# Kernel tuning notes

Measured on AMD Instinct MI355X. Metric: run time of the kernel, lower is better.

Reference implementation:

```python
import jax, jax.numpy as jnp
import numpy as np

N = 30000      # entities
E = 200000     # KG triples
E_ALL = 400000 # full-graph edges
R = 500        # relations
EH = 300       # e_hidden
RH = 100       # r_hidden
H = 8          # GAT / R2E heads
H_E2R = 2      # E2R heads: int(softmax(head_selector).sum()+1) == 2 always
EPS = 1e-16    # torch_geometric softmax eps


def _seg_softmax(logits, idx, num):
    # logits: [E, heads]; segment-wise stable softmax over edges grouped by idx
    m = jax.ops.segment_max(logits, idx, num_segments=num)
    ex = jnp.exp(logits - m[idx])
    s = jax.ops.segment_sum(ex, idx, num_segments=num)
    return ex / (s[idx] + EPS)


def _gcn(x, ei):
    j, i = ei[0], ei[1]
    deg = jax.ops.segment_sum(jnp.ones(ei.shape[1], x.dtype), i, num_segments=N)
    dis = jnp.where(deg > 0, deg ** -0.5, 0.0)
    norm = dis[j] * dis[i]                                        # [E_all]
    agg = jax.ops.segment_sum(norm[:, None] * x[j], i, num_segments=N)
    return jax.nn.relu(agg)


def _highway(x1, x2, w, b):
    gate = jax.nn.sigmoid(x1 @ w.T + b)
    return gate * x2 + (1.0 - gate) * x1


def setup_inputs() -> dict:
    key = jax.random.key(0)
    ks = jax.random.split(key, 20)
    f = jnp.float32
    inp = {
        'x_e': jax.random.normal(ks[0], (N, EH), f),
        'edge_index': jax.random.randint(ks[1], (2, E), 0, N),
        'rel': jax.random.randint(ks[2], (E,), 0, R),
        'edge_index_all': jax.random.randint(ks[3], (2, E_ALL), 0, N),
        'rel_all': jax.random.randint(ks[4], (E_ALL,), 0, R),
        # Highway layers
        'hw1_w': jax.random.normal(ks[5], (EH, EH), f) / np.sqrt(EH),
        'hw1_b': jnp.zeros((EH,), f),
        'hw2_w': jax.random.normal(ks[6], (EH, EH), f) / np.sqrt(EH),
        'hw2_b': jnp.zeros((EH,), f),
        # E2R (only first H_E2R heads are ever used)
        'e2r_wh': jax.random.normal(ks[7], (RH, EH), f) / np.sqrt(EH),
        'e2r_wt': jax.random.normal(ks[8], (RH, EH), f) / np.sqrt(EH),
        'e2r_ah': jax.random.normal(ks[9], (H_E2R, RH), f) / np.sqrt(RH),
        'e2r_at': jax.random.normal(ks[10], (H_E2R, RH), f) / np.sqrt(RH),
        # R2E
        'r2e_ah': jax.random.normal(ks[11], (H, EH), f) / np.sqrt(EH),
        'r2e_at': jax.random.normal(ks[12], (H, EH), f) / np.sqrt(EH),
        'r2e_ar': jax.random.normal(ks[13], (H, RH), f) / np.sqrt(RH),
        # GAT over e_hidden + 2*r_hidden = 500
        'gat_ai': jax.random.normal(ks[14], (H, EH + 2 * RH), f) / np.sqrt(EH + 2 * RH),
        'gat_aj': jax.random.normal(ks[15], (H, EH + 2 * RH), f) / np.sqrt(EH + 2 * RH),
    }
    return inp


def reference(x_e, edge_index, rel, edge_index_all, rel_all,
              hw1_w, hw1_b, hw2_w, hw2_b,
              e2r_wh, e2r_wt, e2r_ah, e2r_at,
              r2e_ah, r2e_at, r2e_ar, gat_ai, gat_aj):
    lrelu = jax.nn.leaky_relu  # slope 0.01, matches torch default

    # --- two GCN + Highway blocks (dropout = identity at eval) ---
    x = _highway(x_e, _gcn(x_e, edge_index_all), hw1_w, hw1_b)
    x = _highway(x, _gcn(x, edge_index_all), hw2_w, hw2_b)

    h_idx, t_idx = edge_index[0], edge_index[1]

    # --- E2R: entity -> relation (2 heads; spmm sum over heads folded into alpha sum) ---
    xh = x @ e2r_wh.T                        # [N, RH]
    xt = x @ e2r_wt.T                        # [N, RH]
    e1 = (xh @ e2r_ah.T)[h_idx] + (xt @ e2r_at.T)[t_idx]   # [E, H_E2R]
    a1 = _seg_softmax(lrelu(e1), rel, R)
    xr_h = jax.ops.segment_sum(a1.sum(1)[:, None] * xh[h_idx], rel, num_segments=R)
    e2 = (xt @ e2r_ah.T)[h_idx] + (xh @ e2r_at.T)[t_idx]
    a2 = _seg_softmax(lrelu(e2), rel, R)
    xr_t = jax.ops.segment_sum(a2.sum(1)[:, None] * xt[t_idx], rel, num_segments=R)
    x_r = (xr_h + xr_t) / H_E2R / 2.0        # [R, RH]

    # --- R2E: relation -> entity (8 heads) ---
    se_h = x @ r2e_ah.T                      # [N, H]
    se_t = x @ r2e_at.T
    sr = x_r @ r2e_ar.T                      # [R, H]
    a_h = _seg_softmax(lrelu(se_h[h_idx] + sr[rel]), h_idx, N)
    a_t = _seg_softmax(lrelu(se_t[t_idx] + sr[rel]), t_idx, N)
    xr_rel = x_r[rel]                        # [E, RH]
    xe_h = jax.ops.segment_sum(a_h.sum(1)[:, None] * xr_rel, h_idx, num_segments=N) / H
    xe_t = jax.ops.segment_sum(a_t.sum(1)[:, None] * xr_rel, t_idx, num_segments=N) / H
    x2 = jnp.concatenate([x, xe_h, xe_t], axis=1)          # [N, EH+2*RH]

    # --- GAT over full graph (8 heads) ---
    j_a, i_a = edge_index_all[0], edge_index_all[1]
    e_ij = (x2 @ gat_ai.T)[i_a] + (x2 @ gat_aj.T)[j_a]     # [E_all, H]
    al = _seg_softmax(lrelu(e_ij), i_a, N)
    x_gat = jax.ops.segment_sum(al.sum(1)[:, None] * x2[j_a], i_a, num_segments=N) / H

    return jnp.concatenate([x2, x_gat], axis=1)            # [N, 2*(EH+2*RH)]
```

## Files before the change

### kernel.cpp

```cpp
#include <hip/hip_runtime.h>
#include <math.h>

constexpr int N_    = 30000;
constexpr int E_    = 200000;
constexpr int EALL_ = 400000;
constexpr int R_    = 500;
constexpr int EH_   = 300;
constexpr int RH_   = 100;
constexpr int X2D_  = 500;
constexpr int OUTD_ = 1000;
constexpr int LD4   = OUTD_/4;
constexpr int EH4   = EH_/4;
constexpr int RH4   = RH_/4;
constexpr int NC_   = 16;
constexpr int XBS_  = 320;
constexpr int XEBS_ = 200;
constexpr int KP_   = 320;
constexpr int NBR_  = 64;
constexpr int PERB_ = (E_ + NBR_ - 1)/NBR_;
constexpr int SCB_  = 2048;
constexpr int NSB_  = (N_ + SCB_ - 1)/SCB_;
constexpr int SCNP_ = NSB_*SCB_;

typedef __attribute__((ext_vector_type(4))) float f32x4;
typedef __attribute__((ext_vector_type(8))) short s16x8;

__device__ __forceinline__ float lrelu_(float v){ return v > 0.f ? v : 0.01f*v; }
__device__ __forceinline__ float sig_(float z){ return 1.f/(1.f + expf(-z)); }
__device__ __forceinline__ unsigned short f2bf_(float f){
  unsigned int u = __float_as_uint(f);
  unsigned int r = (u + 0x7FFFu + ((u >> 16) & 1u)) >> 16;
  return (unsigned short)r;
}
__device__ __forceinline__ float bf2f_(unsigned short h){
  return __uint_as_float(((unsigned int)h) << 16);
}

__global__ void k_count3(const int* __restrict__ ia,
                         const int* __restrict__ hi, const int* __restrict__ ti,
                         int* cd, int* ch, int* ct){
  int idx = blockIdx.x*blockDim.x + threadIdx.x;
  if (idx < EALL_) { atomicAdd(&cd[ia[idx]], 1); return; }
  idx -= EALL_;
  if (idx < E_) { atomicAdd(&ch[hi[idx]], 1); return; }
  idx -= E_;
  if (idx < E_) { atomicAdd(&ct[ti[idx]], 1); return; }
}

__global__ void k_scanA(const int* __restrict__ c0, const int* __restrict__ c1,
                        const int* __restrict__ c2, int* __restrict__ bsum){
  int arr = blockIdx.x / NSB_, b = blockIdx.x - arr*NSB_;
  const int* c = arr == 0 ? c0 : (arr == 1 ? c1 : c2);
  int t = threadIdx.x;
  const int4* c4 = reinterpret_cast<const int4*>(c + b*SCB_ + t*8);
  int4 u0 = c4[0], u1 = c4[1];
  int acc = u0.x+u0.y+u0.z+u0.w + u1.x+u1.y+u1.z+u1.w;
  __shared__ int red[256];
  red[t] = acc;
  __syncthreads();
  for (int o = 128; o > 0; o >>= 1){
    if (t < o) red[t] += red[t+o];
    __syncthreads();
  }
  if (t == 0) bsum[arr*NSB_ + b] = red[0];
}

__global__ void k_scanB(int* __restrict__ bsum, int* o0, int* o1, int* o2){
  int t = threadIdx.x;
  if (t < 3){
    int run = 0;
    for (int b = 0; b < NSB_; ++b){ int v = bsum[t*NSB_ + b]; bsum[t*NSB_ + b] = run; run += v; }
    int* o = t == 0 ? o0 : (t == 1 ? o1 : o2);
    o[N_] = run;
  }
}

__global__ void k_scanC(const int* __restrict__ c0, const int* __restrict__ c1,
                        const int* __restrict__ c2, const int* __restrict__ bsum,
                        int* o0, int* o1, int* o2, float* __restrict__ dis){
  int arr = blockIdx.x / NSB_, b = blockIdx.x - arr*NSB_;
  const int* c = arr == 0 ? c0 : (arr == 1 ? c1 : c2);
  int* o = arr == 0 ? o0 : (arr == 1 ? o1 : o2);
  int t = threadIdx.x;
  int base = b*SCB_ + t*8;
  const int4* c4 = reinterpret_cast<const int4*>(c + base);
  int4 u0 = c4[0], u1 = c4[1];
  int v[8] = {u0.x,u0.y,u0.z,u0.w,u1.x,u1.y,u1.z,u1.w};
  int tot = v[0]+v[1]+v[2]+v[3]+v[4]+v[5]+v[6]+v[7];
  __shared__ int sc[256];
  sc[t] = tot;
  __syncthreads();
  for (int off = 1; off < 256; off <<= 1){
    int add = (t >= off) ? sc[t-off] : 0;
    __syncthreads();
    sc[t] += add;
    __syncthreads();
  }
  int run = bsum[arr*NSB_ + b] + (t ? sc[t-1] : 0);
  #pragma unroll
  for (int i = 0; i < 8; ++i){
    int idx = base + i;
    o[idx] = run;
    if (arr == 0) dis[idx] = v[i] > 0 ? rsqrtf((float)v[i]) : 0.f;
    run += v[i];
  }
}

__global__ void k_scatter3(const int* __restrict__ ja, const int* __restrict__ ia,
                           const int* __restrict__ rel, const int* __restrict__ hi,
                           const int* __restrict__ ti,
                           const int* od, const int* oh, const int* ot,
                           int* curd, int* curh, int* curt,
                           const float* __restrict__ dis,
                           int* j_dest, float* wj,
                           int* relh, int* relt){
  int idx = blockIdx.x*blockDim.x + threadIdx.x;
  if (idx < EALL_){
    int e = idx, s = ia[e];
    int p = od[s] + atomicAdd(&curd[s], 1);
    int j = ja[e];
    j_dest[p] = j; wj[p] = dis[j]; return;
  }
  idx -= EALL_;
  if (idx < E_){
    int e = idx, s = hi[e];
    int p = oh[s] + atomicAdd(&curh[s], 1);
    relh[p] = rel[e]; return;
  }
  idx -= E_;
  if (idx < E_){
    int e = idx, s = ti[e];
    int p = ot[s] + atomicAdd(&curt[s], 1);
    relt[p] = rel[e]; return;
  }
}

__global__ void k_relhist(const int* __restrict__ rel, int* __restrict__ H){
  __shared__ int h[R_];
  int b = blockIdx.x, tid = threadIdx.x;
  for (int i = tid; i < R_; i += 256) h[i] = 0;
  __syncthreads();
  int s = b*PERB_, e = min(s + PERB_, E_);
  for (int i = s + tid; i < e; i += 256) atomicAdd(&h[rel[i]], 1);
  __syncthreads();
  for (int i = tid; i < R_; i += 256) H[b*R_ + i] = h[i];
}

__global__ void k_relscan(int* __restrict__ H, int* __restrict__ off_rel){
  __shared__ int tot[R_];
  __shared__ int sc[256];
  int tid = threadIdx.x;
  for (int r = tid; r < R_; r += 256){
    int acc = 0;
    for (int b = 0; b < NBR_; ++b){ int v = H[b*R_ + r]; H[b*R_ + r] = acc; acc += v; }
    tot[r] = acc;
  }
  __syncthreads();
  int r0 = tid*2;
  int a0 = (r0 < R_) ? tot[r0] : 0;
  int a1 = (r0+1 < R_) ? tot[r0+1] : 0;
  sc[tid] = a0 + a1;
  __syncthreads();
  for (int off = 1; off < 256; off <<= 1){
    int add = (tid >= off) ? sc[tid-off] : 0;
    __syncthreads();
    sc[tid] += add;
    __syncthreads();
  }
  int run = tid ? sc[tid-1] : 0;
  if (r0 < R_)   off_rel[r0]   = run;
  if (r0+1 < R_) off_rel[r0+1] = run + a0;
  if (tid == 255) off_rel[R_] = sc[255];
  __syncthreads();
  for (int r = tid; r < R_; r += 256){
    int o = off_rel[r];
    for (int b = 0; b < NBR_; ++b) H[b*R_ + r] += o;
  }
}

__global__ void k_relscatter(const int* __restrict__ rel, const int* __restrict__ hi,
                             const int* __restrict__ ti, const int* __restrict__ H,
                             int* __restrict__ hr, int* __restrict__ tr){
  __shared__ int cur[R_];
  int b = blockIdx.x, tid = threadIdx.x;
  for (int i = tid; i < R_; i += 256) cur[i] = H[b*R_ + i];
  __syncthreads();
  int s = b*PERB_, e = min(s + PERB_, E_);
  for (int i = s + tid; i < e; i += 256){
    int r = rel[i];
    int p = atomicAdd(&cur[r], 1);
    hr[p] = hi[i]; tr[p] = ti[i];
  }
}

__global__ void k_pack_x(const float4* __restrict__ X, int ldx4,
                         unsigned short* __restrict__ xb){
  int idx = blockIdx.x*blockDim.x + threadIdx.x;
  if (idx >= N_*80) return;
  int n = idx / 80, c = idx - n*80;
  ushort4 o = make_ushort4(0,0,0,0);
  if (c < EH4){
    float4 v = X[(size_t)n*ldx4 + c];
    o.x = f2bf_(v.x); o.y = f2bf_(v.y); o.z = f2bf_(v.z); o.w = f2bf_(v.w);
  }
  *reinterpret_cast<ushort4*>(&xb[(size_t)n*XBS_ + c*4]) = o;
}

__global__ void k_pack_weights(const float* __restrict__ w1, const float* __restrict__ w2,
                               const float* __restrict__ wh, const float* __restrict__ wt,
                               unsigned short* w1b, unsigned short* w2b,
                               unsigned short* wcb){
  int idx = blockIdx.x*blockDim.x + threadIdx.x;
  if (idx < EH_*KP_){
    int n = idx/KP_, k = idx - n*KP_;
    w1b[idx] = (k < EH_) ? f2bf_(w1[(size_t)n*EH_ + k]) : (unsigned short)0;
    return;
  }
  idx -= EH_*KP_;
  if (idx < EH_*KP_){
    int n = idx/KP_, k = idx - n*KP_;
    w2b[idx] = (k < EH_) ? f2bf_(w2[(size_t)n*EH_ + k]) : (unsigned short)0;
    return;
  }
  idx -= EH_*KP_;
  if (idx < 200*KP_){
    int n = idx/KP_, k = idx - n*KP_;
    wcb[idx] = (k < EH_) ? f2bf_((n < 100) ? wh[(size_t)n*EH_ + k] : wt[(size_t)(n-100)*EH_ + k])
                         : (unsigned short)0;
  }
}

__global__ __launch_bounds__(256) void k_gemm_mfma(
    const unsigned short* __restrict__ Ab,
    const unsigned short* __restrict__ Wb,
    float* __restrict__ C, int ldc, int M, int Nn){
  constexpr int WS = 328;
  constexpr int AS = 40;
  __shared__ unsigned short Ws[64*WS];
  __shared__ unsigned short As[128*AS];
  int tid = threadIdx.x;
  int lane = tid & 63, wave = tid >> 6;
  int wm = wave & 1, wn = wave >> 1;
  int m0 = blockIdx.x*128, n0 = blockIdx.y*64;

  for (int c = tid; c < 64*(KP_/8); c += 256){
    int n = c / (KP_/8), k8 = (c % (KP_/8))*8;
    s16x8 v = {0,0,0,0,0,0,0,0};
    if (n0 + n < Nn)
      v = *reinterpret_cast<const s16x8*>(&Wb[(size_t)(n0+n)*KP_ + k8]);
    *reinterpret_cast<s16x8*>(&Ws[n*WS + k8]) = v;
  }

  f32x4 acc[4][2] = {};
  int kf = (lane >> 4)*8;
  int rA = lane & 15;
  for (int k0 = 0; k0 < KP_; k0 += 32){
    __syncthreads();
    for (int c = tid; c < 128*4; c += 256){
      int r = c >> 2, k8 = (c & 3)*8;
      s16x8 v = {0,0,0,0,0,0,0,0};
      if (m0 + r < M)
        v = *reinterpret_cast<const s16x8*>(&Ab[(size_t)(m0+r)*XBS_ + k0 + k8]);
      *reinterpret_cast<s16x8*>(&As[r*AS + k8]) = v;
    }
    __syncthreads();
    s16x8 afr[4], bfr[2];
    #pragma unroll
    for (int mf = 0; mf < 4; ++mf)
      afr[mf] = *reinterpret_cast<const s16x8*>(&As[(wm*64 + mf*16 + rA)*AS + kf]);
    #pragma unroll
    for (int nf = 0; nf < 2; ++nf)
      bfr[nf] = *reinterpret_cast<const s16x8*>(&Ws[(wn*32 + nf*16 + rA)*WS + k0 + kf]);
    #pragma unroll
    for (int mf = 0; mf < 4; ++mf)
      #pragma unroll
      for (int nf = 0; nf < 2; ++nf)
        acc[mf][nf] = __builtin_amdgcn_mfma_f32_16x16x32_bf16(afr[mf], bfr[nf], acc[mf][nf], 0, 0, 0);
  }
  int col0 = n0 + wn*32 + (lane & 15);
  int rbase = m0 + wm*64 + (lane >> 4)*4;
  #pragma unroll
  for (int mf = 0; mf < 4; ++mf){
    #pragma unroll
    for (int nf = 0; nf < 2; ++nf){
      int col = col0 + nf*16;
      if (col < Nn){
        #pragma unroll
        for (int r = 0; r < 4; ++r){
          int row = rbase + mf*16 + r;
          if (row < M) C[(size_t)row*ldc + col] = acc[mf][nf][r];
        }
      }
    }
  }
}

__global__ void k_gcn4(const int* __restrict__ off, const int* __restrict__ jd,
                       const float* __restrict__ wj, const float* __restrict__ dis,
                       const unsigned short* __restrict__ xb, float4* __restrict__ Y){
  __shared__ int js[64];
  __shared__ float ws[64];
  int n = blockIdx.x, lane = threadIdx.x;
  int s = off[n], t = off[n+1];
  bool two = lane < (EH4 - 64);
  float4 a0 = make_float4(0.f,0.f,0.f,0.f);
  float4 a1 = make_float4(0.f,0.f,0.f,0.f);
  for (int base = s; base < t; base += 64){
    int m = min(64, t - base);
    __syncthreads();
    if (lane < m){ js[lane] = jd[base+lane]; ws[lane] = wj[base+lane]; }
    __syncthreads();
    int q = 0;
    for (; q + 1 < m; q += 2){
      size_t r0 = (size_t)js[q]*XBS_, r1 = (size_t)js[q+1]*XBS_;
      float w0 = ws[q], w1 = ws[q+1];
      ushort4 u0 = *reinterpret_cast<const ushort4*>(&xb[r0 + lane*4]);
      ushort4 u1 = *reinterpret_cast<const ushort4*>(&xb[r1 + lane*4]);
      a0.x += w0*bf2f_(u0.x) + w1*bf2f_(u1.x);
      a0.y += w0*bf2f_(u0.y) + w1*bf2f_(u1.y);
      a0.z += w0*bf2f_(u0.z) + w1*bf2f_(u1.z);
      a0.w += w0*bf2f_(u0.w) + w1*bf2f_(u1.w);
      if (two){
        ushort4 v0 = *reinterpret_cast<const ushort4*>(&xb[r0 + 256 + lane*4]);
        ushort4 v1 = *reinterpret_cast<const ushort4*>(&xb[r1 + 256 + lane*4]);
        a1.x += w0*bf2f_(v0.x) + w1*bf2f_(v1.x);
        a1.y += w0*bf2f_(v0.y) + w1*bf2f_(v1.y);
        a1.z += w0*bf2f_(v0.z) + w1*bf2f_(v1.z);
        a1.w += w0*bf2f_(v0.w) + w1*bf2f_(v1.w);
      }
    }
    if (q < m){
      size_t r0 = (size_t)js[q]*XBS_;
      float w0 = ws[q];
      ushort4 u0 = *reinterpret_cast<const ushort4*>(&xb[r0 + lane*4]);
      a0.x += w0*bf2f_(u0.x); a0.y += w0*bf2f_(u0.y);
      a0.z += w0*bf2f_(u0.z); a0.w += w0*bf2f_(u0.w);
      if (two){
        ushort4 v0 = *reinterpret_cast<const ushort4*>(&xb[r0 + 256 + lane*4]);
        a1.x += w0*bf2f_(v0.x); a1.y += w0*bf2f_(v0.y);
        a1.z += w0*bf2f_(v0.z); a1.w += w0*bf2f_(v0.w);
      }
    }
  }
  float dn = dis[n];
  float4 r;
  r.x = fmaxf(dn*a0.x, 0.f); r.y = fmaxf(dn*a0.y, 0.f);
  r.z = fmaxf(dn*a0.z, 0.f); r.w = fmaxf(dn*a0.w, 0.f);
  Y[(size_t)n*EH4 + lane] = r;
  if (two){
    r.x = fmaxf(dn*a1.x, 0.f); r.y = fmaxf(dn*a1.y, 0.f);
    r.z = fmaxf(dn*a1.z, 0.f); r.w = fmaxf(dn*a1.w, 0.f);
    Y[(size_t)n*EH4 + 64 + lane] = r;
  }
}

__global__ void k_highway3(const float4* __restrict__ Xold, int ldo4,
                           const float4* __restrict__ Y, const float4* __restrict__ G,
                           const float* __restrict__ b,
                           float4* __restrict__ Xn, unsigned short* __restrict__ xbb){
  int idx = blockIdx.x*blockDim.x + threadIdx.x;
  if (idx >= N_*EH4) return;
  int n = idx / EH4, f = idx - n*EH4;
  float4 g4 = G[idx];
  float4 b4 = reinterpret_cast<const float4*>(b)[f];
  float4 y4 = Y[idx];
  float4 xo = Xold[(size_t)n*ldo4 + f];
  float4 r;
  float gx;
  gx = sig_(g4.x + b4.x); r.x = gx*y4.x + (1.f-gx)*xo.x;
  gx = sig_(g4.y + b4.y); r.y = gx*y4.y + (1.f-gx)*xo.y;
  gx = sig_(g4.z + b4.z); r.z = gx*y4.z + (1.f-gx)*xo.z;
  gx = sig_(g4.w + b4.w); r.w = gx*y4.w + (1.f-gx)*xo.w;
  Xn[(size_t)n*LD4 + f] = r;
  ushort4 o;
  o.x = f2bf_(r.x); o.y = f2bf_(r.y); o.z = f2bf_(r.z); o.w = f2bf_(r.w);
  *reinterpret_cast<ushort4*>(&xbb[(size_t)n*XBS_ + f*4]) = o;
}

__global__ void k_pproj(const float* __restrict__ xhxt,
                        const float* __restrict__ ah, const float* __restrict__ at,
                        float4* __restrict__ pht){
  int n = blockIdx.x*blockDim.x + threadIdx.x;
  if (n >= N_) return;
  float a0=0,a1=0,b0=0,b1=0,c0=0,c1=0,d0=0,d1=0;
  const float* xh = xhxt + (size_t)n*200;
  const float* xt = xh + 100;
  for (int f = 0; f < RH_; ++f) {
    float vh = xh[f], vt = xt[f];
    float w0 = ah[f], w1 = ah[RH_+f], u0 = at[f], u1 = at[RH_+f];
    a0 += vh*w0; a1 += vh*w1;
    b0 += vt*u0; b1 += vt*u1;
    c0 += vt*w0; c1 += vt*w1;
    d0 += vh*u0; d1 += vh*u1;
  }
  pht[(size_t)n*2]     = make_float4(a0, a1, c0, c1);
  pht[(size_t)n*2 + 1] = make_float4(b0, b1, d0, d1);
}

__global__ void k_fold_rel2(const int* __restrict__ off,
                            const int* __restrict__ hr, const int* __restrict__ tr,
                            const float4* __restrict__ pht,
                            float* __restrict__ s1p, float* __restrict__ s2p){
  __shared__ float4 redm[4];
  __shared__ float4 reds[4];
  int r = blockIdx.x;
  int tid = threadIdx.x, lane = tid & 63, w = tid >> 6;
  int s = off[r], e = off[r+1];
  float4 mx = make_float4(-1e30f,-1e30f,-1e30f,-1e30f);
  for (int p = s + tid; p < e; p += 256){
    float4 ph = pht[(size_t)hr[p]*2];
    float4 pt = pht[(size_t)tr[p]*2 + 1];
    mx.x = fmaxf(mx.x, lrelu_(ph.x + pt.x));
    mx.y = fmaxf(mx.y, lrelu_(ph.y + pt.y));
    mx.z = fmaxf(mx.z, lrelu_(ph.z + pt.z));
    mx.w = fmaxf(mx.w, lrelu_(ph.w + pt.w));
  }
  #pragma unroll
  for (int o = 1; o < 64; o <<= 1){
    mx.x = fmaxf(mx.x, __shfl_xor(mx.x, o));
    mx.y = fmaxf(mx.y, __shfl_xor(mx.y, o));
    mx.z = fmaxf(mx.z, __shfl_xor(mx.z, o));
    mx.w = fmaxf(mx.w, __shfl_xor(mx.w, o));
  }
  if (lane == 0) redm[w] = mx;
  __syncthreads();
  float4 m;
  m.x = fmaxf(fmaxf(redm[0].x, redm[1].x), fmaxf(redm[2].x, redm[3].x));
  m.y = fmaxf(fmaxf(redm[0].y, redm[1].y), fmaxf(redm[2].y, redm[3].y));
  m.z = fmaxf(fmaxf(redm[0].z, redm[1].z), fmaxf(redm[2].z, redm[3].z));
  m.w = fmaxf(fmaxf(redm[0].w, redm[1].w), fmaxf(redm[2].w, redm[3].w));
  float4 sm = make_float4(0.f,0.f,0.f,0.f);
  for (int p = s + tid; p < e; p += 256){
    float4 ph = pht[(size_t)hr[p]*2];
    float4 pt = pht[(size_t)tr[p]*2 + 1];
    sm.x += expf(lrelu_(ph.x + pt.x) - m.x);
    sm.y += expf(lrelu_(ph.y + pt.y) - m.y);
    sm.z += expf(lrelu_(ph.z + pt.z) - m.z);
    sm.w += expf(lrelu_(ph.w + pt.w) - m.w);
  }
  #pragma unroll
  for (int o = 1; o < 64; o <<= 1){
    sm.x += __shfl_xor(sm.x, o);
    sm.y += __shfl_xor(sm.y, o);
    sm.z += __shfl_xor(sm.z, o);
    sm.w += __shfl_xor(sm.w, o);
  }
  if (lane == 0) reds[w] = sm;
  __syncthreads();
  float4 sv;
  sv.x = reds[0].x + reds[1].x + reds[2].x + reds[3].x;
  sv.y = reds[0].y + reds[1].y + reds[2].y + reds[3].y;
  sv.z = reds[0].z + reds[1].z + reds[2].z + reds[3].z;
  sv.w = reds[0].w + reds[1].w + reds[2].w + reds[3].w;
  float4 inv;
  inv.x = 1.f/(sv.x + 1e-16f); inv.y = 1.f/(sv.y + 1e-16f);
  inv.z = 1.f/(sv.z + 1e-16f); inv.w = 1.f/(sv.w + 1e-16f);
  for (int p = s + tid; p < e; p += 256){
    float4 ph = pht[(size_t)hr[p]*2];
    float4 pt = pht[(size_t)tr[p]*2 + 1];
    s1p[p] = expf(lrelu_(ph.x + pt.x) - m.x)*inv.x + expf(lrelu_(ph.y + pt.y) - m.y)*inv.y;
    s2p[p] = expf(lrelu_(ph.z + pt.z) - m.z)*inv.z + expf(lrelu_(ph.w + pt.w) - m.w)*inv.w;
  }
}

__global__ void k_fold_ht2(const int* __restrict__ offh, const int* __restrict__ offt,
                           const int* __restrict__ relh, const int* __restrict__ relt,
                           const float* __restrict__ st16, const float* __restrict__ sr8,
                           float* __restrict__ shp, float* __restrict__ stp){
  int w = threadIdx.x >> 6, lane = threadIdx.x & 63;
  int n = blockIdx.x*2 + (w >> 1);
  if (n >= N_) return;
  int side = w & 1;
  const int* off = side ? offt : offh;
  const int* rl  = side ? relt : relh;
  float* op = side ? stp : shp;
  int k = lane & 7, g = lane >> 3;
  float cst = st16[(size_t)n*16 + side*8 + k];
  int s = off[n], e = off[n+1];
  float m = -1e30f;
  for (int p = s + g; p < e; p += 8)
    m = fmaxf(m, lrelu_(cst + sr8[(size_t)rl[p]*8 + k]));
  #pragma unroll
  for (int o = 8; o < 64; o <<= 1) m = fmaxf(m, __shfl_xor(m, o));
  float sum = 0.f;
  for (int p = s + g; p < e; p += 8)
    sum += expf(lrelu_(cst + sr8[(size_t)rl[p]*8 + k]) - m);
  #pragma unroll
  for (int o = 8; o < 64; o <<= 1) sum += __shfl_xor(sum, o);
  float inv = 1.f / (sum + 1e-16f);
  for (int p = s + g; p < e; p += 8){
    float t = expf(lrelu_(cst + sr8[(size_t)rl[p]*8 + k]) - m) * inv;
    #pragma unroll
    for (int o = 1; o < 8; o <<= 1) t += __shfl_xor(t, o);
    if (k == 0) op[p] = t;
  }
}

__global__ void k_fold_gat2(const int* __restrict__ off, const int* __restrict__ jd,
                            const float* __restrict__ gg16, float* __restrict__ agp){
  int w = threadIdx.x >> 6, lane = threadIdx.x & 63;
  int n = blockIdx.x*4 + w;
  if (n >= N_) return;
  int k = lane & 7, g = lane >> 3;
  float cst = gg16[(size_t)n*16 + k];
  int s = off[n], e = off[n+1];
  float m = -1e30f;
  for (int p = s + g; p < e; p += 8)
    m = fmaxf(m, lrelu_(cst + gg16[(size_t)jd[p]*16 + 8 + k]));
  #pragma unroll
  for (int o = 8; o < 64; o <<= 1) m = fmaxf(m, __shfl_xor(m, o));
  float sum = 0.f;
  for (int p = s + g; p < e; p += 8)
    sum += expf(lrelu_(cst + gg16[(size_t)jd[p]*16 + 8 + k]) - m);
  #pragma unroll
  for (int o = 8; o < 64; o <<= 1) sum += __shfl_xor(sum, o);
  float inv = 1.f / (sum + 1e-16f);
  for (int p = s + g; p < e; p += 8){
    float t = expf(lrelu_(cst + gg16[(size_t)jd[p]*16 + 8 + k]) - m) * inv;
    #pragma unroll
    for (int o = 1; o < 8; o <<= 1) t += __shfl_xor(t, o);
    if (k == 0) agp[p] = t;
  }
}

__global__ void k_e2r_agg3(const int* __restrict__ off,
                           const int* __restrict__ hr, const int* __restrict__ tr,
                           const float* __restrict__ s1p, const float* __restrict__ s2p,
                           const float4* __restrict__ xhxt4, float4* __restrict__ xr_part){
  int r = blockIdx.x, c = blockIdx.y;
  int lane = threadIdx.x;
  int side = lane >> 5, fl = lane & 31;
  int s = off[r], e = off[r+1];
  int len = e - s;
  int per = (len + NC_ - 1)/NC_;
  int cs = s + c*per, ce = min(cs + per, e);
  float4 acc = make_float4(0.f,0.f,0.f,0.f);
  if (fl < RH4){
    const int* idx = side ? tr : hr;
    const float* wv = side ? s2p : s1p;
    int fofs = side ? 25 + fl : fl;
    int p = cs;
    for (; p + 1 < ce; p += 2){
      float a0 = wv[p], a1 = wv[p+1];
      float4 v0 = xhxt4[(size_t)idx[p]*50 + fofs];
      float4 v1 = xhxt4[(size_t)idx[p+1]*50 + fofs];
      acc.x += a0*v0.x + a1*v1.x; acc.y += a0*v0.y + a1*v1.y;
      acc.z += a0*v0.z + a1*v1.z; acc.w += a0*v0.w + a1*v1.w;
    }
    if (p < ce){
      float a0 = wv[p];
      float4 v0 = xhxt4[(size_t)idx[p]*50 + fofs];
      acc.x += a0*v0.x; acc.y += a0*v0.y; acc.z += a0*v0.z; acc.w += a0*v0.w;
    }
  }
  float4 oth;
  oth.x = __shfl_xor(acc.x, 32); oth.y = __shfl_xor(acc.y, 32);
  oth.z = __shfl_xor(acc.z, 32); oth.w = __shfl_xor(acc.w, 32);
  if (side == 0 && fl < RH4){
    float4 o = make_float4(acc.x+oth.x, acc.y+oth.y, acc.z+oth.z, acc.w+oth.w);
    xr_part[((size_t)c*R_ + r)*RH4 + fl] = o;
  }
}

__global__ void k_e2r_red2(const float4* __restrict__ xr_part, float4* __restrict__ xr4,
                           const float* __restrict__ ar, float* __restrict__ sr8){
  __shared__ float row[RH_];
  int r = blockIdx.x, lane = threadIdx.x;
  if (lane < RH4){
    float4 a = make_float4(0.f,0.f,0.f,0.f);
    #pragma unroll
    for (int c = 0; c < NC_; ++c){
      float4 v = xr_part[((size_t)c*R_ + r)*RH4 + lane];
      a.x += v.x; a.y += v.y; a.z += v.z; a.w += v.w;
    }
    a.x *= 0.25f; a.y *= 0.25f; a.z *= 0.25f; a.w *= 0.25f;
    xr4[(size_t)r*RH4 + lane] = a;
    row[lane*4]   = a.x; row[lane*4+1] = a.y;
    row[lane*4+2] = a.z; row[lane*4+3] = a.w;
  }
  __syncthreads();
  int h = lane & 7, gk = lane >> 3;
  float acc = 0.f;
  for (int k = gk; k < RH_; k += 8) acc += row[k]*ar[(size_t)h*RH_ + k];
  #pragma unroll
  for (int o = 8; o < 64; o <<= 1) acc += __shfl_xor(acc, o);
  if (lane < 8) sr8[(size_t)r*8 + lane] = acc;
}

__global__ void k_dots16(const float* __restrict__ X, int ldx, int K,
                         const float* __restrict__ wA, const float* __restrict__ wB,
                         float* __restrict__ out16, int M){
  __shared__ float xs[16][65];
  __shared__ float ws[16][65];
  int tid = threadIdx.x;
  int tx = tid & 15, ty = tid >> 4;
  int r0 = blockIdx.x*16;
  float acc = 0.f;
  for (int c0 = 0; c0 < K; c0 += 64){
    int cl = min(64, K - c0);
    #pragma unroll
    for (int i = 0; i < 4; ++i){
      int idx = tid + i*256;
      int r = idx >> 6, k = idx & 63;
      float xv = 0.f, wv = 0.f;
      if (k < cl && r0 + r < M) xv = X[(size_t)(r0+r)*ldx + c0 + k];
      if (k < cl) wv = (r < 8) ? wA[(size_t)r*K + c0 + k] : wB[(size_t)(r-8)*K + c0 + k];
      xs[r][k] = xv;
      ws[r][k] = wv;
    }
    __syncthreads();
    #pragma unroll
    for (int k = 0; k < 64; ++k) acc += xs[ty][k]*ws[tx][k];
    __syncthreads();
  }
  if (r0 + ty < M) out16[(size_t)(r0+ty)*16 + tx] = acc;
}

__global__ void k_r2e_agg2b(const int* __restrict__ offh, const int* __restrict__ offt,
                            const int* __restrict__ relh, const int* __restrict__ relt,
                            const float* __restrict__ shp, const float* __restrict__ stp,
                            const float4* __restrict__ xr4, float4* __restrict__ out,
                            unsigned short* __restrict__ xeb){
  int n = blockIdx.x;
  int side = threadIdx.x >> 6, lane = threadIdx.x & 63;
  const int* off = side ? offt : offh;
  const int* rr  = side ? relt : relh;
  const float* sp = side ? stp : shp;
  int s = off[n], e = off[n+1];
  if (lane >= RH4) return;
  float4 acc = make_float4(0.f,0.f,0.f,0.f);
  int p = s;
  for (; p + 1 < e; p += 2){
    float a0 = sp[p], a1 = sp[p+1];
    float4 v0 = xr4[(size_t)rr[p]*RH4 + lane];
    float4 v1 = xr4[(size_t)rr[p+1]*RH4 + lane];
    acc.x += a0*v0.x + a1*v1.x; acc.y += a0*v0.y + a1*v1.y;
    acc.z += a0*v0.z + a1*v1.z; acc.w += a0*v0.w + a1*v1.w;
  }
  if (p < e){
    float a0 = sp[p];
    float4 v0 = xr4[(size_t)rr[p]*RH4 + lane];
    acc.x += a0*v0.x; acc.y += a0*v0.y; acc.z += a0*v0.z; acc.w += a0*v0.w;
  }
  float4 o = make_float4(acc.x*0.125f, acc.y*0.125f, acc.z*0.125f, acc.w*0.125f);
  out[(size_t)n*LD4 + (side ? 100 : 75) + lane] = o;
  ushort4 ob;
  ob.x = f2bf_(o.x); ob.y = f2bf_(o.y); ob.z = f2bf_(o.z); ob.w = f2bf_(o.w);
  *reinterpret_cast<ushort4*>(&xeb[(size_t)n*XEBS_ + (side ? 100 : 0) + lane*4]) = ob;
}

__global__ void k_gat_agg4(const int* __restrict__ off, const int* __restrict__ jd,
                           const float* __restrict__ agp,
                           const unsigned short* __restrict__ xb,
                           const unsigned short* __restrict__ xeb,
                           float4* __restrict__ out){
  __shared__ int js[128];
  __shared__ float as_[128];
  int n = blockIdx.x, tid = threadIdx.x;
  int s = off[n], t = off[n+1];
  const unsigned short* tbl;
  size_t stride; int cofs;
  if (tid < 75){ tbl = xb;  stride = XBS_;  cofs = tid*4; }
  else         { tbl = xeb; stride = XEBS_; cofs = (tid-75)*4; }
  float4 acc = make_float4(0.f,0.f,0.f,0.f);
  for (int base = s; base < t; base += 128){
    int m = min(128, t - base);
    __syncthreads();
    if (tid < m){ js[tid] = jd[base+tid]; as_[tid] = agp[base+tid]; }
    __syncthreads();
    if (tid < 125){
      int q = 0;
      for (; q + 1 < m; q += 2){
        float a0 = as_[q], a1 = as_[q+1];
        ushort4 u0 = *reinterpret_cast<const ushort4*>(&tbl[(size_t)js[q]*stride + cofs]);
        ushort4 u1 = *reinterpret_cast<const ushort4*>(&tbl[(size_t)js[q+1]*stride + cofs]);
        acc.x += a0*bf2f_(u0.x) + a1*bf2f_(u1.x);
        acc.y += a0*bf2f_(u0.y) + a1*bf2f_(u1.y);
        acc.z += a0*bf2f_(u0.z) + a1*bf2f_(u1.z);
        acc.w += a0*bf2f_(u0.w) + a1*bf2f_(u1.w);
      }
      if (q < m){
        float a0 = as_[q];
        ushort4 u0 = *reinterpret_cast<const ushort4*>(&tbl[(size_t)js[q]*stride + cofs]);
        acc.x += a0*bf2f_(u0.x); acc.y += a0*bf2f_(u0.y);
        acc.z += a0*bf2f_(u0.z); acc.w += a0*bf2f_(u0.w);
      }
    }
  }
  if (tid < 125){
    float4 r = make_float4(acc.x*0.125f, acc.y*0.125f, acc.z*0.125f, acc.w*0.125f);
    out[(size_t)n*LD4 + 125 + tid] = r;
  }
}

static inline void gemm_mfma(const unsigned short* Ab, const unsigned short* Wb,
                             float* C, int ldc, int M, int Nn, hipStream_t st){
  dim3 g((M + 127)/128, (Nn + 63)/64);
  k_gemm_mfma<<<g, 256, 0, st>>>(Ab, Wb, C, ldc, M, Nn);
}

extern "C" void kernel_launch(void* const* d_in, const int* in_sizes, int n_in,
                              void* d_out, int out_size, void* d_ws, size_t ws_size,
                              hipStream_t stream) {
  const float* x_e   = (const float*)d_in[0];
  const int*   ei    = (const int*)d_in[1];
  const int*   rel   = (const int*)d_in[2];
  const int*   eia   = (const int*)d_in[3];
  const float* hw1_w = (const float*)d_in[5];
  const float* hw1_b = (const float*)d_in[6];
  const float* hw2_w = (const float*)d_in[7];
  const float* hw2_b = (const float*)d_in[8];
  const float* e2r_wh= (const float*)d_in[9];
  const float* e2r_wt= (const float*)d_in[10];
  const float* e2r_ah= (const float*)d_in[11];
  const float* e2r_at= (const float*)d_in[12];
  const float* r2e_ah= (const float*)d_in[13];
  const float* r2e_at= (const float*)d_in[14];
  const float* r2e_ar= (const float*)d_in[15];
  const float* gat_ai= (const float*)d_in[16];
  const float* gat_aj= (const float*)d_in[17];
  float* out = (float*)d_out;

  const int* hi = ei;
  const int* ti = ei + E_;
  const int* ja = eia;
  const int* ia = eia + EALL_;

  char* base = (char*)d_ws;
  size_t off = 0;
  auto alloc = [&](size_t bytes)->void*{
    void* p = base + off;
    off = (off + bytes + 255) & ~(size_t)255;
    return p;
  };

  size_t z0 = off;
  int* cnt_dest = (int*)alloc(SCNP_*4);
  int* cnt_h    = (int*)alloc(SCNP_*4);
  int* cnt_t    = (int*)alloc(SCNP_*4);
  int* cur_dest = (int*)alloc(N_*4);
  int* cur_h    = (int*)alloc(N_*4);
  int* cur_t    = (int*)alloc(N_*4);
  size_t z1 = off;

  int* off_dest = (int*)alloc(SCNP_*4);
  int* off_h    = (int*)alloc(SCNP_*4);
  int* off_t    = (int*)alloc(SCNP_*4);
  int* off_rel  = (int*)alloc((R_+1)*4);
  int* bsum     = (int*)alloc(3*NSB_*4);
  int* Hrel     = (int*)alloc((size_t)NBR_*R_*4);
  int* j_dest   = (int*)alloc((size_t)EALL_*4);
  int* hr       = (int*)alloc((size_t)E_*4);
  int* tr       = (int*)alloc((size_t)E_*4);
  int* relh     = (int*)alloc((size_t)E_*4);
  int* relt     = (int*)alloc((size_t)E_*4);

  float* dis   = (float*)alloc(SCNP_*4);
  float* wj    = (float*)alloc((size_t)EALL_*4);
  float* y     = (float*)alloc((size_t)N_*EH_*4);
  float* g     = (float*)alloc((size_t)N_*EH_*4);
  float* xhxt  = (float*)alloc((size_t)N_*200*4);
  float* pht   = (float*)alloc((size_t)N_*8*4);
  float* s1p   = (float*)alloc((size_t)E_*4);
  float* s2p   = (float*)alloc((size_t)E_*4);
  float* xr    = (float*)alloc((size_t)R_*RH_*4);
  float* xr_part=(float*)alloc((size_t)NC_*R_*RH_*4);
  float* st16  = (float*)alloc((size_t)N_*16*4);
  float* sr8   = (float*)alloc((size_t)R_*8*4);
  float* shp   = (float*)alloc((size_t)E_*4);
  float* stp   = (float*)alloc((size_t)E_*4);
  float* gg16  = (float*)alloc((size_t)N_*16*4);
  float* agp   = (float*)alloc((size_t)EALL_*4);
  unsigned short* xb  = (unsigned short*)alloc((size_t)N_*XBS_*2);
  unsigned short* xeb = (unsigned short*)alloc((size_t)N_*XEBS_*2);
  unsigned short* w1b = (unsigned short*)alloc((size_t)EH_*KP_*2);
  unsigned short* w2b = (unsigned short*)alloc((size_t)EH_*KP_*2);
  unsigned short* wcb = (unsigned short*)alloc((size_t)200*KP_*2);

  hipMemsetAsync(base + z0, 0, z1 - z0, stream);

  const int TB = 256;
  const int TOT = EALL_ + 2*E_;
  int gTOT  = (TOT + TB - 1)/TB;
  int gN    = (N_ + TB - 1)/TB;
  int gPKX  = (N_*80 + TB - 1)/TB;
  const int WTOT = 2*EH_*KP_ + 200*KP_;

  k_pack_weights<<<(WTOT + TB - 1)/TB, TB, 0, stream>>>(hw1_w, hw2_w, e2r_wh, e2r_wt,
                                                        w1b, w2b, wcb);

  k_relhist<<<NBR_, 256, 0, stream>>>(rel, Hrel);
  k_relscan<<<1, 256, 0, stream>>>(Hrel, off_rel);
  k_relscatter<<<NBR_, 256, 0, stream>>>(rel, hi, ti, Hrel, hr, tr);

  k_count3<<<gTOT, TB, 0, stream>>>(ia, hi, ti, cnt_dest, cnt_h, cnt_t);
  k_scanA<<<3*NSB_, 256, 0, stream>>>(cnt_dest, cnt_h, cnt_t, bsum);
  k_scanB<<<1, 64, 0, stream>>>(bsum, off_dest, off_h, off_t);
  k_scanC<<<3*NSB_, 256, 0, stream>>>(cnt_dest, cnt_h, cnt_t, bsum,
                                      off_dest, off_h, off_t, dis);
  k_scatter3<<<gTOT, TB, 0, stream>>>(ja, ia, rel, hi, ti,
                                      off_dest, off_h, off_t,
                                      cur_dest, cur_h, cur_t,
                                      dis, j_dest, wj, relh, relt);

  k_pack_x<<<gPKX, TB, 0, stream>>>((const float4*)x_e, EH4, xb);
  gemm_mfma(xb, w1b, g, EH_, N_, EH_, stream);
  k_gcn4<<<N_, 64, 0, stream>>>(off_dest, j_dest, wj, dis, xb, (float4*)y);
  k_highway3<<<(N_*EH4 + TB - 1)/TB, TB, 0, stream>>>((const float4*)x_e, EH4, (const float4*)y,
                                                      (const float4*)g, hw1_b, (float4*)out, xb);
  gemm_mfma(xb, w2b, g, EH_, N_, EH_, stream);
  k_gcn4<<<N_, 64, 0, stream>>>(off_dest, j_dest, wj, dis, xb, (float4*)y);
  k_highway3<<<(N_*EH4 + TB - 1)/TB, TB, 0, stream>>>((const float4*)out, LD4, (const float4*)y,
                                                      (const float4*)g, hw2_b, (float4*)out, xb);

  gemm_mfma(xb, wcb, xhxt, 200, N_, 200, stream);
  k_pproj<<<gN, TB, 0, stream>>>(xhxt, e2r_ah, e2r_at, (float4*)pht);
  k_fold_rel2<<<R_, 256, 0, stream>>>(off_rel, hr, tr, (const float4*)pht, s1p, s2p);
  k_e2r_agg3<<<dim3(R_, NC_), 64, 0, stream>>>(off_rel, hr, tr, s1p, s2p,
                                               (const float4*)xhxt, (float4*)xr_part);
  k_e2r_red2<<<R_, 64, 0, stream>>>((const float4*)xr_part, (float4*)xr, r2e_ar, sr8);

  k_dots16<<<(N_+15)/16, 256, 0, stream>>>(out, OUTD_, EH_, r2e_ah, r2e_at, st16, N_);
  k_fold_ht2<<<(N_+1)/2, 256, 0, stream>>>(off_h, off_t, relh, relt, st16, sr8, shp, stp);
  k_r2e_agg2b<<<N_, 128, 0, stream>>>(off_h, off_t, relh, relt, shp, stp,
                                      (const float4*)xr, (float4*)out, xeb);

  k_dots16<<<(N_+15)/16, 256, 0, stream>>>(out, OUTD_, X2D_, gat_ai, gat_aj, gg16, N_);
  k_fold_gat2<<<(N_+3)/4, 256, 0, stream>>>(off_dest, j_dest, gg16, agp);
  k_gat_agg4<<<N_, 128, 0, stream>>>(off_dest, j_dest, agp, xb, xeb, (float4*)out);
}
```

Measured before the change: 651.8 us.

## Fuse highway gate into GCN gather and feed score dots from bf16 copies

The highway gating and bf16 repack are folded into the GCN aggregation kernel, so the intermediate y buffer is no longer written and re-read. Ping-pong bf16 buffers avoid overwriting the gather source in place. The per-row attention score dot kernels now read the bf16 activation copies instead of fp32 rows, with the GAT dots split into two accumulating passes. Gather loops are unrolled by four for more memory parallelism. Scores now come from bf16-rounded inputs, which slightly changes numerics.

```diff
diff --git a/kernel.cpp b/kernel.cpp
--- a/kernel.cpp
+++ b/kernel.cpp
@@ -7,7 +7,6 @@
 constexpr int R_    = 500;
 constexpr int EH_   = 300;
 constexpr int RH_   = 100;
-constexpr int X2D_  = 500;
 constexpr int OUTD_ = 1000;
 constexpr int LD4   = OUTD_/4;
 constexpr int EH4   = EH_/4;
@@ -295,9 +294,12 @@
   }
 }
 
-__global__ void k_gcn4(const int* __restrict__ off, const int* __restrict__ jd,
+__global__ void k_gcn5(const int* __restrict__ off, const int* __restrict__ jd,
                        const float* __restrict__ wj, const float* __restrict__ dis,
-                       const unsigned short* __restrict__ xb, float4* __restrict__ Y){
+                       const unsigned short* __restrict__ xsrc,
+                       const float4* __restrict__ Xold, int ldo4,
+                       const float4* __restrict__ G, const float* __restrict__ b,
+                       float4* __restrict__ Xn, unsigned short* __restrict__ xdst){
   __shared__ int js[64];
   __shared__ float ws[64];
   int n = blockIdx.x, lane = threadIdx.x;
@@ -311,70 +313,82 @@
     if (lane < m){ js[lane] = jd[base+lane]; ws[lane] = wj[base+lane]; }
     __syncthreads();
     int q = 0;
-    for (; q + 1 < m; q += 2){
-      size_t r0 = (size_t)js[q]*XBS_, r1 = (size_t)js[q+1]*XBS_;
-      float w0 = ws[q], w1 = ws[q+1];
-      ushort4 u0 = *reinterpret_cast<const ushort4*>(&xb[r0 + lane*4]);
-      ushort4 u1 = *reinterpret_cast<const ushort4*>(&xb[r1 + lane*4]);
-      a0.x += w0*bf2f_(u0.x) + w1*bf2f_(u1.x);
-      a0.y += w0*bf2f_(u0.y) + w1*bf2f_(u1.y);
-      a0.z += w0*bf2f_(u0.z) + w1*bf2f_(u1.z);
-      a0.w += w0*bf2f_(u0.w) + w1*bf2f_(u1.w);
+    for (; q + 3 < m; q += 4){
+      size_t r0 = (size_t)js[q]*XBS_,   r1 = (size_t)js[q+1]*XBS_;
+      size_t r2 = (size_t)js[q+2]*XBS_, r3 = (size_t)js[q+3]*XBS_;
+      float w0 = ws[q], w1 = ws[q+1], w2 = ws[q+2], w3 = ws[q+3];
+      ushort4 u0 = *reinterpret_cast<const ushort4*>(&xsrc[r0 + lane*4]);
+      ushort4 u1 = *reinterpret_cast<const ushort4*>(&xsrc[r1 + lane*4]);
+      ushort4 u2 = *reinterpret_cast<const ushort4*>(&xsrc[r2 + lane*4]);
+      ushort4 u3 = *reinterpret_cast<const ushort4*>(&xsrc[r3 + lane*4]);
+      a0.x += w0*bf2f_(u0.x)+w1*bf2f_(u1.x)+w2*bf2f_(u2.x)+w3*bf2f_(u3.x);
+      a0.y += w0*bf2f_(u0.y)+w1*bf2f_(u1.y)+w2*bf2f_(u2.y)+w3*bf2f_(u3.y);
+      a0.z += w0*bf2f_(u0.z)+w1*bf2f_(u1.z)+w2*bf2f_(u2.z)+w3*bf2f_(u3.z);
+      a0.w += w0*bf2f_(u0.w)+w1*bf2f_(u1.w)+w2*bf2f_(u2.w)+w3*bf2f_(u3.w);
       if (two){
-        ushort4 v0 = *reinterpret_cast<const ushort4*>(&xb[r0 + 256 + lane*4]);
-        ushort4 v1 = *reinterpret_cast<const ushort4*>(&xb[r1 + 256 + lane*4]);
-        a1.x += w0*bf2f_(v0.x) + w1*bf2f_(v1.x);
-        a1.y += w0*bf2f_(v0.y) + w1*bf2f_(v1.y);
-        a1.z += w0*bf2f_(v0.z) + w1*bf2f_(v1.z);
-        a1.w += w0*bf2f_(v0.w) + w1*bf2f_(v1.w);
+        ushort4 v0 = *reinterpret_cast<const ushort4*>(&xsrc[r0 + 256 + lane*4]);
+        ushort4 v1 = *reinterpret_cast<const ushort4*>(&xsrc[r1 + 256 + lane*4]);
+        ushort4 v2 = *reinterpret_cast<const ushort4*>(&xsrc[r2 + 256 + lane*4]);
+        ushort4 v3 = *reinterpret_cast<const ushort4*>(&xsrc[r3 + 256 + lane*4]);
+        a1.x += w0*bf2f_(v0.x)+w1*bf2f_(v1.x)+w2*bf2f_(v2.x)+w3*bf2f_(v3.x);
+        a1.y += w0*bf2f_(v0.y)+w1*bf2f_(v1.y)+w2*bf2f_(v2.y)+w3*bf2f_(v3.y);
+        a1.z += w0*bf2f_(v0.z)+w1*bf2f_(v1.z)+w2*bf2f_(v2.z)+w3*bf2f_(v3.z);
+        a1.w += w0*bf2f_(v0.w)+w1*bf2f_(v1.w)+w2*bf2f_(v2.w)+w3*bf2f_(v3.w);
       }
     }
-    if (q < m){
+    for (; q < m; ++q){
       size_t r0 = (size_t)js[q]*XBS_;
       float w0 = ws[q];
-      ushort4 u0 = *reinterpret_cast<const ushort4*>(&xb[r0 + lane*4]);
+      ushort4 u0 = *reinterpret_cast<const ushort4*>(&xsrc[r0 + lane*4]);
       a0.x += w0*bf2f_(u0.x); a0.y += w0*bf2f_(u0.y);
       a0.z += w0*bf2f_(u0.z); a0.w += w0*bf2f_(u0.w);
       if (two){
-        ushort4 v0 = *reinterpret_cast<const ushort4*>(&xb[r0 + 256 + lane*4]);
+        ushort4 v0 = *reinterpret_cast<const ushort4*>(&xsrc[r0 + 256 + lane*4]);
         a1.x += w0*bf2f_(v0.x); a1.y += w0*bf2f_(v0.y);
         a1.z += w0*bf2f_(v0.z); a1.w += w0*bf2f_(v0.w);
       }
     }
   }
   float dn = dis[n];
-  float4 r;
-  r.x = fmaxf(dn*a0.x, 0.f); r.y = fmaxf(dn*a0.y, 0.f);
-  r.z = fmaxf(dn*a0.z, 0.f); r.w = fmaxf(dn*a0.w, 0.f);
-  Y[(size_t)n*EH4 + lane] = r;
+  {
+    int c = lane;
+    float4 yv;
+    yv.x = fmaxf(dn*a0.x, 0.f); yv.y = fmaxf(dn*a0.y, 0.f);
+    yv.z = fmaxf(dn*a0.z, 0.f); yv.w = fmaxf(dn*a0.w, 0.f);
+    float4 g4 = G[(size_t)n*EH4 + c];
+    float4 b4 = reinterpret_cast<const float4*>(b)[c];
+    float4 xo = Xold[(size_t)n*ldo4 + c];
+    float gx; float4 r;
+    gx = sig_(g4.x + b4.x); r.x = gx*yv.x + (1.f-gx)*xo.x;
+    gx = sig_(g4.y + b4.y); r.y = gx*yv.y + (1.f-gx)*xo.y;
+    gx = sig_(g4.z + b4.z); r.z = gx*yv.z + (1.f-gx)*xo.z;
+    gx = sig_(g4.w + b4.w); r.w = gx*yv.w + (1.f-gx)*xo.w;
+    Xn[(size_t)n*LD4 + c] = r;
+    ushort4 o;
+    o.x = f2bf_(r.x); o.y = f2bf_(r.y); o.z = f2bf_(r.z); o.w = f2bf_(r.w);
+    *reinterpret_cast<ushort4*>(&xdst[(size_t)n*XBS_ + c*4]) = o;
+  }
   if (two){
-    r.x = fmaxf(dn*a1.x, 0.f); r.y = fmaxf(dn*a1.y, 0.f);
-    r.z = fmaxf(dn*a1.z, 0.f); r.w = fmaxf(dn*a1.w, 0.f);
-    Y[(size_t)n*EH4 + 64 + lane] = r;
-  }
-}
-
-__global__ void k_highway3(const float4* __restrict__ Xold, int ldo4,
-                           const float4* __restrict__ Y, const float4* __restrict__ G,
-                           const float* __restrict__ b,
-                           float4* __restrict__ Xn, unsigned short* __restrict__ xbb){
-  int idx = blockIdx.x*blockDim.x + threadIdx.x;
-  if (idx >= N_*EH4) return;
-  int n = idx / EH4, f = idx - n*EH4;
-  float4 g4 = G[idx];
-  float4 b4 = reinterpret_cast<const float4*>(b)[f];
-  float4 y4 = Y[idx];
-  float4 xo = Xold[(size_t)n*ldo4 + f];
-  float4 r;
-  float gx;
-  gx = sig_(g4.x + b4.x); r.x = gx*y4.x + (1.f-gx)*xo.x;
-  gx = sig_(g4.y + b4.y); r.y = gx*y4.y + (1.f-gx)*xo.y;
-  gx = sig_(g4.z + b4.z); r.z = gx*y4.z + (1.f-gx)*xo.z;
-  gx = sig_(g4.w + b4.w); r.w = gx*y4.w + (1.f-gx)*xo.w;
-  Xn[(size_t)n*LD4 + f] = r;
-  ushort4 o;
-  o.x = f2bf_(r.x); o.y = f2bf_(r.y); o.z = f2bf_(r.z); o.w = f2bf_(r.w);
-  *reinterpret_cast<ushort4*>(&xbb[(size_t)n*XBS_ + f*4]) = o;
+    int c = 64 + lane;
+    float4 yv;
+    yv.x = fmaxf(dn*a1.x, 0.f); yv.y = fmaxf(dn*a1.y, 0.f);
+    yv.z = fmaxf(dn*a1.z, 0.f); yv.w = fmaxf(dn*a1.w, 0.f);
+    float4 g4 = G[(size_t)n*EH4 + c];
+    float4 b4 = reinterpret_cast<const float4*>(b)[c];
+    float4 xo = Xold[(size_t)n*ldo4 + c];
+    float gx; float4 r;
+    gx = sig_(g4.x + b4.x); r.x = gx*yv.x + (1.f-gx)*xo.x;
+    gx = sig_(g4.y + b4.y); r.y = gx*yv.y + (1.f-gx)*xo.y;
+    gx = sig_(g4.z + b4.z); r.z = gx*yv.z + (1.f-gx)*xo.z;
+    gx = sig_(g4.w + b4.w); r.w = gx*yv.w + (1.f-gx)*xo.w;
+    Xn[(size_t)n*LD4 + c] = r;
+    ushort4 o;
+    o.x = f2bf_(r.x); o.y = f2bf_(r.y); o.z = f2bf_(r.z); o.w = f2bf_(r.w);
+    *reinterpret_cast<ushort4*>(&xdst[(size_t)n*XBS_ + c*4]) = o;
+  } else if (lane < 16){
+    ushort4 z = make_ushort4(0,0,0,0);
+    *reinterpret_cast<ushort4*>(&xdst[(size_t)n*XBS_ + (64+lane)*4]) = z;
+  }
 }
 
 __global__ void k_pproj(const float* __restrict__ xhxt,
@@ -587,33 +601,41 @@
   if (lane < 8) sr8[(size_t)r*8 + lane] = acc;
 }
 
-__global__ void k_dots16(const float* __restrict__ X, int ldx, int K,
-                         const float* __restrict__ wA, const float* __restrict__ wB,
-                         float* __restrict__ out16, int M){
+__global__ void k_dots16b(const unsigned short* __restrict__ X, int ldx, int K, int colofs, int Kw,
+                          const float* __restrict__ wA, const float* __restrict__ wB,
+                          float* __restrict__ out16, int M, int accum){
   __shared__ float xs[16][65];
   __shared__ float ws[16][65];
   int tid = threadIdx.x;
   int tx = tid & 15, ty = tid >> 4;
   int r0 = blockIdx.x*16;
+  int lr = tid >> 4;
+  int lc = (tid & 15)*4;
   float acc = 0.f;
   for (int c0 = 0; c0 < K; c0 += 64){
     int cl = min(64, K - c0);
-    #pragma unroll
-    for (int i = 0; i < 4; ++i){
-      int idx = tid + i*256;
-      int r = idx >> 6, k = idx & 63;
-      float xv = 0.f, wv = 0.f;
-      if (k < cl && r0 + r < M) xv = X[(size_t)(r0+r)*ldx + c0 + k];
-      if (k < cl) wv = (r < 8) ? wA[(size_t)r*K + c0 + k] : wB[(size_t)(r-8)*K + c0 + k];
-      xs[r][k] = xv;
-      ws[r][k] = wv;
-    }
+    float4 xv = make_float4(0.f,0.f,0.f,0.f);
+    if (r0 + lr < M && lc < cl){
+      ushort4 u = *reinterpret_cast<const ushort4*>(&X[(size_t)(r0+lr)*ldx + c0 + lc]);
+      xv.x = bf2f_(u.x); xv.y = bf2f_(u.y); xv.z = bf2f_(u.z); xv.w = bf2f_(u.w);
+    }
+    float4 wv = make_float4(0.f,0.f,0.f,0.f);
+    if (lc < cl){
+      const float* wsrc = (lr < 8) ? &wA[(size_t)lr*Kw + colofs + c0 + lc]
+                                   : &wB[(size_t)(lr-8)*Kw + colofs + c0 + lc];
+      wv = *reinterpret_cast<const float4*>(wsrc);
+    }
+    xs[lr][lc] = xv.x; xs[lr][lc+1] = xv.y; xs[lr][lc+2] = xv.z; xs[lr][lc+3] = xv.w;
+    ws[lr][lc] = wv.x; ws[lr][lc+1] = wv.y; ws[lr][lc+2] = wv.z; ws[lr][lc+3] = wv.w;
     __syncthreads();
     #pragma unroll
     for (int k = 0; k < 64; ++k) acc += xs[ty][k]*ws[tx][k];
     __syncthreads();
   }
-  if (r0 + ty < M) out16[(size_t)(r0+ty)*16 + tx] = acc;
+  if (r0 + ty < M){
+    size_t o = (size_t)(r0+ty)*16 + tx;
+    out16[o] = accum ? out16[o] + acc : acc;
+  }
 }
 
 __global__ void k_r2e_agg2b(const int* __restrict__ offh, const int* __restrict__ offt,
@@ -670,16 +692,18 @@
     __syncthreads();
     if (tid < 125){
       int q = 0;
-      for (; q + 1 < m; q += 2){
-        float a0 = as_[q], a1 = as_[q+1];
+      for (; q + 3 < m; q += 4){
+        float a0 = as_[q], a1 = as_[q+1], a2 = as_[q+2], a3 = as_[q+3];
         ushort4 u0 = *reinterpret_cast<const ushort4*>(&tbl[(size_t)js[q]*stride + cofs]);
         ushort4 u1 = *reinterpret_cast<const ushort4*>(&tbl[(size_t)js[q+1]*stride + cofs]);
-        acc.x += a0*bf2f_(u0.x) + a1*bf2f_(u1.x);
-        acc.y += a0*bf2f_(u0.y) + a1*bf2f_(u1.y);
-        acc.z += a0*bf2f_(u0.z) + a1*bf2f_(u1.z);
-        acc.w += a0*bf2f_(u0.w) + a1*bf2f_(u1.w);
+        ushort4 u2 = *reinterpret_cast<const ushort4*>(&tbl[(size_t)js[q+2]*stride + cofs]);
+        ushort4 u3 = *reinterpret_cast<const ushort4*>(&tbl[(size_t)js[q+3]*stride + cofs]);
+        acc.x += a0*bf2f_(u0.x)+a1*bf2f_(u1.x)+a2*bf2f_(u2.x)+a3*bf2f_(u3.x);
+        acc.y += a0*bf2f_(u0.y)+a1*bf2f_(u1.y)+a2*bf2f_(u2.y)+a3*bf2f_(u3.y);
+        acc.z += a0*bf2f_(u0.z)+a1*bf2f_(u1.z)+a2*bf2f_(u2.z)+a3*bf2f_(u3.z);
+        acc.w += a0*bf2f_(u0.w)+a1*bf2f_(u1.w)+a2*bf2f_(u2.w)+a3*bf2f_(u3.w);
       }
-      if (q < m){
+      for (; q < m; ++q){
         float a0 = as_[q];
         ushort4 u0 = *reinterpret_cast<const ushort4*>(&tbl[(size_t)js[q]*stride + cofs]);
         acc.x += a0*bf2f_(u0.x); acc.y += a0*bf2f_(u0.y);
@@ -757,7 +781,6 @@
 
   float* dis   = (float*)alloc(SCNP_*4);
   float* wj    = (float*)alloc((size_t)EALL_*4);
-  float* y     = (float*)alloc((size_t)N_*EH_*4);
   float* g     = (float*)alloc((size_t)N_*EH_*4);
   float* xhxt  = (float*)alloc((size_t)N_*200*4);
   float* pht   = (float*)alloc((size_t)N_*8*4);
@@ -771,7 +794,8 @@
   float* stp   = (float*)alloc((size_t)E_*4);
   float* gg16  = (float*)alloc((size_t)N_*16*4);
   float* agp   = (float*)alloc((size_t)EALL_*4);
-  unsigned short* xb  = (unsigned short*)alloc((size_t)N_*XBS_*2);
+  unsigned short* xbA = (unsigned short*)alloc((size_t)N_*XBS_*2);
+  unsigned short* xbB = (unsigned short*)alloc((size_t)N_*XBS_*2);
   unsigned short* xeb = (unsigned short*)alloc((size_t)N_*XEBS_*2);
   unsigned short* w1b = (unsigned short*)alloc((size_t)EH_*KP_*2);
   unsigned short* w2b = (unsigned short*)alloc((size_t)EH_*KP_*2);
@@ -803,29 +827,30 @@
                                       cur_dest, cur_h, cur_t,
                                       dis, j_dest, wj, relh, relt);
 
-  k_pack_x<<<gPKX, TB, 0, stream>>>((const float4*)x_e, EH4, xb);
-  gemm_mfma(xb, w1b, g, EH_, N_, EH_, stream);
-  k_gcn4<<<N_, 64, 0, stream>>>(off_dest, j_dest, wj, dis, xb, (float4*)y);
-  k_highway3<<<(N_*EH4 + TB - 1)/TB, TB, 0, stream>>>((const float4*)x_e, EH4, (const float4*)y,
-                                                      (const float4*)g, hw1_b, (float4*)out, xb);
-  gemm_mfma(xb, w2b, g, EH_, N_, EH_, stream);
-  k_gcn4<<<N_, 64, 0, stream>>>(off_dest, j_dest, wj, dis, xb, (float4*)y);
-  k_highway3<<<(N_*EH4 + TB - 1)/TB, TB, 0, stream>>>((const float4*)out, LD4, (const float4*)y,
-                                                      (const float4*)g, hw2_b, (float4*)out, xb);
-
-  gemm_mfma(xb, wcb, xhxt, 200, N_, 200, stream);
+  k_pack_x<<<gPKX, TB, 0, stream>>>((const float4*)x_e, EH4, xbA);
+  gemm_mfma(xbA, w1b, g, EH_, N_, EH_, stream);
+  k_gcn5<<<N_, 64, 0, stream>>>(off_dest, j_dest, wj, dis, xbA,
+                                (const float4*)x_e, EH4, (const float4*)g, hw1_b,
+                                (float4*)out, xbB);
+  gemm_mfma(xbB, w2b, g, EH_, N_, EH_, stream);
+  k_gcn5<<<N_, 64, 0, stream>>>(off_dest, j_dest, wj, dis, xbB,
+                                (const float4*)out, LD4, (const float4*)g, hw2_b,
+                                (float4*)out, xbA);
+
+  gemm_mfma(xbA, wcb, xhxt, 200, N_, 200, stream);
   k_pproj<<<gN, TB, 0, stream>>>(xhxt, e2r_ah, e2r_at, (float4*)pht);
   k_fold_rel2<<<R_, 256, 0, stream>>>(off_rel, hr, tr, (const float4*)pht, s1p, s2p);
   k_e2r_agg3<<<dim3(R_, NC_), 64, 0, stream>>>(off_rel, hr, tr, s1p, s2p,
                                                (const float4*)xhxt, (float4*)xr_part);
   k_e2r_red2<<<R_, 64, 0, stream>>>((const float4*)xr_part, (float4*)xr, r2e_ar, sr8);
 
-  k_dots16<<<(N_+15)/16, 256, 0, stream>>>(out, OUTD_, EH_, r2e_ah, r2e_at, st16, N_);
+  k_dots16b<<<(N_+15)/16, 256, 0, stream>>>(xbA, XBS_, EH_, 0, EH_, r2e_ah, r2e_at, st16, N_, 0);
   k_fold_ht2<<<(N_+1)/2, 256, 0, stream>>>(off_h, off_t, relh, relt, st16, sr8, shp, stp);
   k_r2e_agg2b<<<N_, 128, 0, stream>>>(off_h, off_t, relh, relt, shp, stp,
                                       (const float4*)xr, (float4*)out, xeb);
 
-  k_dots16<<<(N_+15)/16, 256, 0, stream>>>(out, OUTD_, X2D_, gat_ai, gat_aj, gg16, N_);
+  k_dots16b<<<(N_+15)/16, 256, 0, stream>>>(xbA, XBS_, EH_, 0, 500, gat_ai, gat_aj, gg16, N_, 0);
+  k_dots16b<<<(N_+15)/16, 256, 0, stream>>>(xeb, XEBS_, 200, EH_, 500, gat_ai, gat_aj, gg16, N_, 1);
   k_fold_gat2<<<(N_+3)/4, 256, 0, stream>>>(off_dest, j_dest, gg16, agp);
-  k_gat_agg4<<<N_, 128, 0, stream>>>(off_dest, j_dest, agp, xb, xeb, (float4*)out);
-}
+  k_gat_agg4<<<N_, 128, 0, stream>>>(off_dest, j_dest, agp, xbA, xeb, (float4*)out);
+}
```

Measured after the change: 624.9 us. 4.1% less time.
